# Kernel optimization log

Measured on AMD Instinct MI355X. Metric: run time of the kernel, lower is better.

Reference implementation:

```python
import jax, jax.numpy as jnp
import numpy as np

NEG = -1.0e9

def setup_inputs() -> dict:
    key = jax.random.key(0)
    kq, kk, kv = jax.random.split(key, 3)
    B, Sq, Sk, D = 8, 2048, 2048, 128
    q = jax.random.normal(kq, (B, Sq, D), dtype=jnp.float32)
    k = jax.random.normal(kk, (B, Sk, D), dtype=jnp.float32)
    v = jax.random.normal(kv, (B, Sk, D), dtype=jnp.float32)
    mask = jnp.ones((B, Sq, Sk), dtype=jnp.int32)  # 1 = attend
    return {"q": q, "k": k, "v": v, "mask": mask}

def reference(q, k, v, mask):
    # scaled scores: [B, Sq, Sk]
    temper = jnp.sqrt(jnp.asarray(k.shape[-1], dtype=q.dtype))
    attn = jnp.einsum('bqd,bkd->bqk', q, k) / temper
    # additive mask: -1e9 where mask == 0
    attn = attn + NEG * (1.0 - mask.astype(attn.dtype))
    attn = jax.nn.softmax(attn, axis=-1)
    # dropout rate 0.0 -> identity
    out = jnp.einsum('bqk,bkd->bqd', attn, v)
    return out, attn
```

## Files before the change

### kernel.cpp

```cpp
#include <hip/hip_runtime.h>
#include <hip/hip_bf16.h>

#define BB 8
#define SQ 2048
#define SK 2048
#define DD 128
#define INV_TEMPER 0.08838834764831845f

using s16x8 = __attribute__((ext_vector_type(8))) short;
using f32x4 = __attribute__((ext_vector_type(4))) float;

__device__ __forceinline__ unsigned short f2bf(float f) {
  union { float f; unsigned u; } v; v.f = f;
  unsigned r = v.u + 0x7FFFu + ((v.u >> 16) & 1u);
  return (unsigned short)(r >> 16);
}
__device__ __forceinline__ float bf2f(unsigned short h) {
  union { unsigned u; float f; } v; v.u = ((unsigned)h) << 16; return v.f;
}

__global__ __launch_bounds__(256) void prep_k_kernel(const float* __restrict__ k,
                                                     unsigned short* __restrict__ kb) {
  const size_t i = ((size_t)blockIdx.x * 256 + threadIdx.x) * 8;
  const float4 a = *(const float4*)(k + i);
  const float4 c = *(const float4*)(k + i + 4);
  ushort4 o0, o1;
  o0.x = f2bf(a.x); o0.y = f2bf(a.y); o0.z = f2bf(a.z); o0.w = f2bf(a.w);
  o1.x = f2bf(c.x); o1.y = f2bf(c.y); o1.z = f2bf(c.z); o1.w = f2bf(c.w);
  *(ushort4*)(kb + i) = o0;
  *(ushort4*)(kb + i + 4) = o1;
}

__global__ __launch_bounds__(256) void prep_v_kernel(const float* __restrict__ v,
                                                     unsigned short* __restrict__ vt) {
  constexpr int TS = 132;
  __shared__ __align__(16) unsigned short tile[64 * TS];
  const int tid = threadIdx.x;
  const int bid = blockIdx.x;
  const int b  = bid >> 5;
  const int k0 = (bid & 31) << 6;
#pragma unroll
  for (int p = 0; p < 8; ++p) {
    const int row = p * 8 + (tid >> 5);
    const int c4  = (tid & 31) << 2;
    const float4 vv = *(const float4*)(v + ((size_t)(b * SK + k0 + row)) * DD + c4);
    ushort4 o; o.x = f2bf(vv.x); o.y = f2bf(vv.y); o.z = f2bf(vv.z); o.w = f2bf(vv.w);
    *(ushort4*)(&tile[row * TS + c4]) = o;
  }
  __syncthreads();
#pragma unroll
  for (int p = 0; p < 8; ++p) {
    const int u = p * 256 + tid;
    const int d  = u >> 4;
    const int kw = (u & 15) << 2;
    ushort4 o;
    o.x = tile[(kw + 0) * TS + d];
    o.y = tile[(kw + 1) * TS + d];
    o.z = tile[(kw + 2) * TS + d];
    o.w = tile[(kw + 3) * TS + d];
    *(ushort4*)(vt + ((size_t)(b * DD + d)) * SK + k0 + kw) = o;
  }
}

__global__ __launch_bounds__(512, 4) void fused_attn(
    const float* __restrict__ q, const int* __restrict__ mask,
    const unsigned short* __restrict__ kb, const unsigned short* __restrict__ vt,
    float* __restrict__ outp, float* __restrict__ attn) {
  constexpr int BMS = 516;
  constexpr int LDP = 136;
  __shared__ unsigned char bm[32 * BMS];
  __shared__ __align__(16) unsigned short p_lds[2][32][LDP];
  __shared__ float redl[8][32];

  const int tid = threadIdx.x;
  const int bid = blockIdx.x;
  const int swz = ((bid & 7) << 6) + (bid >> 3);
  const int b  = swz >> 6;
  const int q0 = (swz & 63) << 5;
  const int lane = tid & 63;
  const int w    = tid >> 6;
  const int lrow = lane & 15;
  const int lk   = lane >> 4;
  const int colw = (w << 4) + lrow;
  const int shq  = colw & 3;

  {
    const int* mbase = mask + ((size_t)(b * SQ + q0)) * SK;
#pragma unroll
    for (int i = 0; i < 32; ++i) {
      const int u = i * 512 + tid;
      const int grow = u >> 9;
      const int gc4  = u & 511;
      const int4 mv = *(const int4*)(mbase + (size_t)grow * SK + ((size_t)gc4 << 2));
      unsigned char nib = (unsigned char)((mv.x != 0) | ((mv.y != 0) << 1) |
                                          ((mv.z != 0) << 2) | ((mv.w != 0) << 3));
      bm[grow * BMS + gc4] = nib;
    }
  }

  s16x8 afrag[2][4];
#pragma unroll
  for (int rt = 0; rt < 2; ++rt) {
    const float* qp = q + ((size_t)(b * SQ + q0 + rt * 16 + lrow)) * DD + lk * 8;
#pragma unroll
    for (int ks = 0; ks < 4; ++ks) {
      const float4 f0 = *(const float4*)(qp + ks * 32);
      const float4 f1 = *(const float4*)(qp + ks * 32 + 4);
      s16x8 a;
      a[0] = (short)f2bf(f0.x); a[1] = (short)f2bf(f0.y);
      a[2] = (short)f2bf(f0.z); a[3] = (short)f2bf(f0.w);
      a[4] = (short)f2bf(f1.x); a[5] = (short)f2bf(f1.y);
      a[6] = (short)f2bf(f1.z); a[7] = (short)f2bf(f1.w);
      afrag[rt][ks] = a;
    }
  }

  const unsigned short* kbb = kb + (size_t)b * SK * DD + (size_t)colw * DD + lk * 8;

  __syncthreads();

  float lsum[2][4];
#pragma unroll
  for (int rt = 0; rt < 2; ++rt)
#pragma unroll
    for (int r = 0; r < 4; ++r) lsum[rt][r] = 0.0f;

#pragma unroll 1
  for (int t = 0; t < 16; ++t) {
    const int kr0 = t << 7;
    s16x8 bfr[4];
#pragma unroll
    for (int ks = 0; ks < 4; ++ks)
      bfr[ks] = *(const s16x8*)(kbb + (size_t)kr0 * DD + ks * 32);
    f32x4 acc[2];
    acc[0] = f32x4{0.f, 0.f, 0.f, 0.f};
    acc[1] = f32x4{0.f, 0.f, 0.f, 0.f};
#pragma unroll
    for (int ks = 0; ks < 4; ++ks) {
      acc[0] = __builtin_amdgcn_mfma_f32_16x16x32_bf16(afrag[0][ks], bfr[ks], acc[0], 0, 0, 0);
      acc[1] = __builtin_amdgcn_mfma_f32_16x16x32_bf16(afrag[1][ks], bfr[ks], acc[1], 0, 0, 0);
    }
#pragma unroll
    for (int rt = 0; rt < 2; ++rt)
#pragma unroll
      for (int r = 0; r < 4; ++r) {
        const int row = rt * 16 + (lk << 2) + r;
        const int live = (bm[row * BMS + (t << 5) + (colw >> 2)] >> shq) & 1;
        const float s = acc[rt][r] * INV_TEMPER;
        lsum[rt][r] += live ? __expf(s) : 0.0f;
      }
  }

#pragma unroll
  for (int rt = 0; rt < 2; ++rt)
#pragma unroll
    for (int r = 0; r < 4; ++r) {
      float l = lsum[rt][r];
#pragma unroll
      for (int d = 1; d < 16; d <<= 1) l += __shfl_xor(l, d);
      lsum[rt][r] = l;
    }
  if (lrow == 0) {
#pragma unroll
    for (int rt = 0; rt < 2; ++rt)
#pragma unroll
      for (int r = 0; r < 4; ++r)
        redl[w][rt * 16 + (lk << 2) + r] = lsum[rt][r];
  }
  __syncthreads();
  float IL[2][4];
#pragma unroll
  for (int rt = 0; rt < 2; ++rt)
#pragma unroll
    for (int r = 0; r < 4; ++r) {
      const int row = rt * 16 + (lk << 2) + r;
      float l = 0.0f;
#pragma unroll
      for (int ww = 0; ww < 8; ++ww) l += redl[ww][row];
      IL[rt][r] = 1.0f / l;
    }

  f32x4 oacc[2];
  oacc[0] = f32x4{0.f, 0.f, 0.f, 0.f};
  oacc[1] = f32x4{0.f, 0.f, 0.f, 0.f};
  const unsigned short* vrow = vt + ((size_t)(b * DD + colw)) * SK + lk * 8;
  const int arow  = tid >> 4;
  const int acol0 = (tid & 15) << 3;
  float* attn_base = attn + ((size_t)(b * SQ + q0 + arow)) * SK + acol0;

#pragma unroll 1
  for (int t = 0; t < 16; ++t) {
    const int kr0 = t << 7;
    const int buf = t & 1;
    s16x8 bfr[4];
#pragma unroll
    for (int ks = 0; ks < 4; ++ks)
      bfr[ks] = *(const s16x8*)(kbb + (size_t)kr0 * DD + ks * 32);
    f32x4 acc[2];
    acc[0] = f32x4{0.f, 0.f, 0.f, 0.f};
    acc[1] = f32x4{0.f, 0.f, 0.f, 0.f};
#pragma unroll
    for (int ks = 0; ks < 4; ++ks) {
      acc[0] = __builtin_amdgcn_mfma_f32_16x16x32_bf16(afrag[0][ks], bfr[ks], acc[0], 0, 0, 0);
      acc[1] = __builtin_amdgcn_mfma_f32_16x16x32_bf16(afrag[1][ks], bfr[ks], acc[1], 0, 0, 0);
    }
#pragma unroll
    for (int rt = 0; rt < 2; ++rt)
#pragma unroll
      for (int r = 0; r < 4; ++r) {
        const int row = rt * 16 + (lk << 2) + r;
        const int live = (bm[row * BMS + (t << 5) + (colw >> 2)] >> shq) & 1;
        const float s = acc[rt][r] * INV_TEMPER;
        const float p = live ? __expf(s) * IL[rt][r] : 0.0f;
        p_lds[buf][row][colw] = f2bf(p);
      }
    __syncthreads();
    {
      const s16x8 pr = *(const s16x8*)(&p_lds[buf][arow][acol0]);
      float4 o0, o1;
      o0.x = bf2f((unsigned short)pr[0]); o0.y = bf2f((unsigned short)pr[1]);
      o0.z = bf2f((unsigned short)pr[2]); o0.w = bf2f((unsigned short)pr[3]);
      o1.x = bf2f((unsigned short)pr[4]); o1.y = bf2f((unsigned short)pr[5]);
      o1.z = bf2f((unsigned short)pr[6]); o1.w = bf2f((unsigned short)pr[7]);
      *(float4*)(attn_base + kr0) = o0;
      *(float4*)(attn_base + kr0 + 4) = o1;
    }
#pragma unroll
    for (int ks = 0; ks < 4; ++ks) {
      const s16x8 pa0 = *(const s16x8*)(&p_lds[buf][lrow][ks * 32 + lk * 8]);
      const s16x8 pa1 = *(const s16x8*)(&p_lds[buf][16 + lrow][ks * 32 + lk * 8]);
      const s16x8 bv = *(const s16x8*)(vrow + kr0 + ks * 32);
      oacc[0] = __builtin_amdgcn_mfma_f32_16x16x32_bf16(pa0, bv, oacc[0], 0, 0, 0);
      oacc[1] = __builtin_amdgcn_mfma_f32_16x16x32_bf16(pa1, bv, oacc[1], 0, 0, 0);
    }
  }

#pragma unroll
  for (int rt = 0; rt < 2; ++rt)
#pragma unroll
    for (int r = 0; r < 4; ++r) {
      const int row = q0 + rt * 16 + (lk << 2) + r;
      outp[((size_t)(b * SQ + row)) * DD + colw] = oacc[rt][r];
    }
}

extern "C" void kernel_launch(void* const* d_in, const int* in_sizes, int n_in,
                              void* d_out, int out_size, void* d_ws, size_t ws_size,
                              hipStream_t stream) {
  const float* q = (const float*)d_in[0];
  const float* k = (const float*)d_in[1];
  const float* v = (const float*)d_in[2];
  const int* mask = (const int*)d_in[3];
  float* outp = (float*)d_out;
  float* attn = outp + (size_t)BB * SQ * DD;

  unsigned short* kb = (unsigned short*)d_ws;
  unsigned short* vt = kb + (size_t)BB * SK * DD;

  prep_k_kernel<<<(BB * SK * DD) / (256 * 8), 256, 0, stream>>>(k, kb);
  prep_v_kernel<<<BB * (SK / 64), 256, 0, stream>>>(v, vt);
  fused_attn<<<BB * (SQ / 32), 512, 0, stream>>>(q, mask, kb, vt, outp, attn);
}
```

Baseline: 141.9 us.

## Prefetch K/V fragments with register double buffering and compact mask to bits

The mask is packed one bit per key instead of a nibble per 4 keys, which halves the LDS bitmap size. Both passes now double-buffer the K fragments in registers so the next tile's global load overlaps the current MFMAs, and V fragments are loaded before the QK MFMAs. The block barrier is replaced by a raw lgkmcnt wait plus s_barrier, and MFMA sections are wrapped in s_setprio. Register pressure rises under the 512x4 launch bounds, which could cause spills.

```diff
diff --git a/kernel.cpp b/kernel.cpp
--- a/kernel.cpp
+++ b/kernel.cpp
@@ -17,6 +17,10 @@
 }
 __device__ __forceinline__ float bf2f(unsigned short h) {
   union { unsigned u; float f; } v; v.u = ((unsigned)h) << 16; return v.f;
+}
+__device__ __forceinline__ void bar_lds() {
+  asm volatile("s_waitcnt lgkmcnt(0)" ::: "memory");
+  __builtin_amdgcn_s_barrier();
 }
 
 __global__ __launch_bounds__(256) void prep_k_kernel(const float* __restrict__ k,
@@ -66,7 +70,7 @@
     const float* __restrict__ q, const int* __restrict__ mask,
     const unsigned short* __restrict__ kb, const unsigned short* __restrict__ vt,
     float* __restrict__ outp, float* __restrict__ attn) {
-  constexpr int BMS = 516;
+  constexpr int BMS = 260;
   constexpr int LDP = 136;
   __shared__ unsigned char bm[32 * BMS];
   __shared__ __align__(16) unsigned short p_lds[2][32][LDP];
@@ -82,165 +86,190 @@
   const int lrow = lane & 15;
   const int lk   = lane >> 4;
   const int colw = (w << 4) + lrow;
-  const int shq  = colw & 3;
+  const int cbyte = colw >> 3;
+  const int cbit  = colw & 7;
+  const int rowb  = lk << 2;
 
   {
     const int* mbase = mask + ((size_t)(b * SQ + q0)) * SK;
 #pragma unroll
-    for (int i = 0; i < 32; ++i) {
-      const int u = i * 512 + tid;
-      const int grow = u >> 9;
-      const int gc4  = u & 511;
-      const int4 mv = *(const int4*)(mbase + (size_t)grow * SK + ((size_t)gc4 << 2));
-      unsigned char nib = (unsigned char)((mv.x != 0) | ((mv.y != 0) << 1) |
-                                          ((mv.z != 0) << 2) | ((mv.w != 0) << 3));
-      bm[grow * BMS + gc4] = nib;
-    }
-  }
-
-  s16x8 afrag[2][4];
-#pragma unroll
-  for (int rt = 0; rt < 2; ++rt) {
-    const float* qp = q + ((size_t)(b * SQ + q0 + rt * 16 + lrow)) * DD + lk * 8;
+    for (int i = 0; i < 16; ++i) {
+      const int u = (i << 9) + tid;
+      const int grow = u >> 8;
+      const int gb   = u & 255;
+      const int* pp = mbase + (size_t)grow * SK + ((size_t)gb << 3);
+      const int4 m0 = *(const int4*)pp;
+      const int4 m1 = *(const int4*)(pp + 4);
+      unsigned bv = (unsigned)(m0.x != 0) | ((unsigned)(m0.y != 0) << 1) |
+                    ((unsigned)(m0.z != 0) << 2) | ((unsigned)(m0.w != 0) << 3) |
+                    ((unsigned)(m1.x != 0) << 4) | ((unsigned)(m1.y != 0) << 5) |
+                    ((unsigned)(m1.z != 0) << 6) | ((unsigned)(m1.w != 0) << 7);
+      bm[grow * BMS + gb] = (unsigned char)bv;
+    }
+  }
+
+  s16x8 af0[4], af1[4];
+#pragma unroll
+  for (int ks = 0; ks < 4; ++ks) {
+    const float* qp0 = q + ((size_t)(b * SQ + q0 + lrow)) * DD + ks * 32 + lk * 8;
+    const float* qp1 = qp0 + 16 * DD;
+    const float4 a0 = *(const float4*)qp0;
+    const float4 a1 = *(const float4*)(qp0 + 4);
+    const float4 c0 = *(const float4*)qp1;
+    const float4 c1 = *(const float4*)(qp1 + 4);
+    s16x8 x, y;
+    x[0] = (short)f2bf(a0.x); x[1] = (short)f2bf(a0.y); x[2] = (short)f2bf(a0.z); x[3] = (short)f2bf(a0.w);
+    x[4] = (short)f2bf(a1.x); x[5] = (short)f2bf(a1.y); x[6] = (short)f2bf(a1.z); x[7] = (short)f2bf(a1.w);
+    y[0] = (short)f2bf(c0.x); y[1] = (short)f2bf(c0.y); y[2] = (short)f2bf(c0.z); y[3] = (short)f2bf(c0.w);
+    y[4] = (short)f2bf(c1.x); y[5] = (short)f2bf(c1.y); y[6] = (short)f2bf(c1.z); y[7] = (short)f2bf(c1.w);
+    af0[ks] = x; af1[ks] = y;
+  }
+
+  const unsigned short* kbb = kb + (size_t)b * SK * DD + (size_t)colw * DD + lk * 8;
+
+  bar_lds();
+
+  float ls[8];
+#pragma unroll
+  for (int i = 0; i < 8; ++i) ls[i] = 0.0f;
+
+  s16x8 bA[4], bB[4];
+#pragma unroll
+  for (int ks = 0; ks < 4; ++ks) bA[ks] = *(const s16x8*)(kbb + ks * 32);
+
+  auto qk_sink1 = [&](int t, const f32x4& a0, const f32x4& a1) {
+    const int bybase = (t << 4) + cbyte;
+#pragma unroll
+    for (int rt = 0; rt < 2; ++rt)
+#pragma unroll
+      for (int r = 0; r < 4; ++r) {
+        const int row = rt * 16 + rowb + r;
+        const int live = (bm[row * BMS + bybase] >> cbit) & 1;
+        const float s = (rt ? a1[r] : a0[r]) * INV_TEMPER;
+        ls[rt * 4 + r] += live ? __expf(s) : 0.0f;
+      }
+  };
+  auto qk_mfma = [&](const s16x8* bf, f32x4& a0, f32x4& a1) {
+    __builtin_amdgcn_s_setprio(1);
 #pragma unroll
     for (int ks = 0; ks < 4; ++ks) {
-      const float4 f0 = *(const float4*)(qp + ks * 32);
-      const float4 f1 = *(const float4*)(qp + ks * 32 + 4);
-      s16x8 a;
-      a[0] = (short)f2bf(f0.x); a[1] = (short)f2bf(f0.y);
-      a[2] = (short)f2bf(f0.z); a[3] = (short)f2bf(f0.w);
-      a[4] = (short)f2bf(f1.x); a[5] = (short)f2bf(f1.y);
-      a[6] = (short)f2bf(f1.z); a[7] = (short)f2bf(f1.w);
-      afrag[rt][ks] = a;
-    }
-  }
-
-  const unsigned short* kbb = kb + (size_t)b * SK * DD + (size_t)colw * DD + lk * 8;
-
-  __syncthreads();
-
-  float lsum[2][4];
-#pragma unroll
-  for (int rt = 0; rt < 2; ++rt)
-#pragma unroll
-    for (int r = 0; r < 4; ++r) lsum[rt][r] = 0.0f;
+      a0 = __builtin_amdgcn_mfma_f32_16x16x32_bf16(af0[ks], bf[ks], a0, 0, 0, 0);
+      a1 = __builtin_amdgcn_mfma_f32_16x16x32_bf16(af1[ks], bf[ks], a1, 0, 0, 0);
+    }
+    __builtin_amdgcn_s_setprio(0);
+  };
 
 #pragma unroll 1
-  for (int t = 0; t < 16; ++t) {
-    const int kr0 = t << 7;
-    s16x8 bfr[4];
-#pragma unroll
-    for (int ks = 0; ks < 4; ++ks)
-      bfr[ks] = *(const s16x8*)(kbb + (size_t)kr0 * DD + ks * 32);
-    f32x4 acc[2];
-    acc[0] = f32x4{0.f, 0.f, 0.f, 0.f};
-    acc[1] = f32x4{0.f, 0.f, 0.f, 0.f};
-#pragma unroll
-    for (int ks = 0; ks < 4; ++ks) {
-      acc[0] = __builtin_amdgcn_mfma_f32_16x16x32_bf16(afrag[0][ks], bfr[ks], acc[0], 0, 0, 0);
-      acc[1] = __builtin_amdgcn_mfma_f32_16x16x32_bf16(afrag[1][ks], bfr[ks], acc[1], 0, 0, 0);
-    }
-#pragma unroll
-    for (int rt = 0; rt < 2; ++rt)
-#pragma unroll
-      for (int r = 0; r < 4; ++r) {
-        const int row = rt * 16 + (lk << 2) + r;
-        const int live = (bm[row * BMS + (t << 5) + (colw >> 2)] >> shq) & 1;
-        const float s = acc[rt][r] * INV_TEMPER;
-        lsum[rt][r] += live ? __expf(s) : 0.0f;
-      }
-  }
-
-#pragma unroll
-  for (int rt = 0; rt < 2; ++rt)
-#pragma unroll
-    for (int r = 0; r < 4; ++r) {
-      float l = lsum[rt][r];
-#pragma unroll
-      for (int d = 1; d < 16; d <<= 1) l += __shfl_xor(l, d);
-      lsum[rt][r] = l;
-    }
+  for (int tp = 0; tp < 8; ++tp) {
+    const int t0 = tp << 1, t1 = t0 + 1;
+    {
+      const unsigned short* p = kbb + (size_t)t1 * (128 * DD);
+#pragma unroll
+      for (int ks = 0; ks < 4; ++ks) bB[ks] = *(const s16x8*)(p + ks * 32);
+    }
+    f32x4 a0 = {0.f,0.f,0.f,0.f}, a1 = {0.f,0.f,0.f,0.f};
+    qk_mfma(bA, a0, a1);
+    qk_sink1(t0, a0, a1);
+    {
+      const int tn = (t0 + 2) & 15;
+      const unsigned short* p = kbb + (size_t)tn * (128 * DD);
+#pragma unroll
+      for (int ks = 0; ks < 4; ++ks) bA[ks] = *(const s16x8*)(p + ks * 32);
+    }
+    f32x4 c0 = {0.f,0.f,0.f,0.f}, c1 = {0.f,0.f,0.f,0.f};
+    qk_mfma(bB, c0, c1);
+    qk_sink1(t1, c0, c1);
+  }
+
+#pragma unroll
+  for (int i = 0; i < 8; ++i) {
+    float l = ls[i];
+#pragma unroll
+    for (int d = 1; d < 16; d <<= 1) l += __shfl_xor(l, d);
+    ls[i] = l;
+  }
   if (lrow == 0) {
 #pragma unroll
-    for (int rt = 0; rt < 2; ++rt)
-#pragma unroll
-      for (int r = 0; r < 4; ++r)
-        redl[w][rt * 16 + (lk << 2) + r] = lsum[rt][r];
-  }
-  __syncthreads();
-  float IL[2][4];
-#pragma unroll
-  for (int rt = 0; rt < 2; ++rt)
-#pragma unroll
-    for (int r = 0; r < 4; ++r) {
-      const int row = rt * 16 + (lk << 2) + r;
-      float l = 0.0f;
-#pragma unroll
-      for (int ww = 0; ww < 8; ++ww) l += redl[ww][row];
-      IL[rt][r] = 1.0f / l;
-    }
-
-  f32x4 oacc[2];
-  oacc[0] = f32x4{0.f, 0.f, 0.f, 0.f};
-  oacc[1] = f32x4{0.f, 0.f, 0.f, 0.f};
+    for (int i = 0; i < 8; ++i) redl[w][(i >> 2) * 16 + rowb + (i & 3)] = ls[i];
+  }
+#pragma unroll
+  for (int ks = 0; ks < 4; ++ks) bA[ks] = *(const s16x8*)(kbb + ks * 32);
+  bar_lds();
+  float il[8];
+#pragma unroll
+  for (int i = 0; i < 8; ++i) {
+    const int row = (i >> 2) * 16 + rowb + (i & 3);
+    float l = 0.0f;
+#pragma unroll
+    for (int ww = 0; ww < 8; ++ww) l += redl[ww][row];
+    il[i] = 1.0f / l;
+  }
+
+  f32x4 o0 = {0.f,0.f,0.f,0.f}, o1 = {0.f,0.f,0.f,0.f};
   const unsigned short* vrow = vt + ((size_t)(b * DD + colw)) * SK + lk * 8;
   const int arow  = tid >> 4;
   const int acol0 = (tid & 15) << 3;
   float* attn_base = attn + ((size_t)(b * SQ + q0 + arow)) * SK + acol0;
 
-#pragma unroll 1
-  for (int t = 0; t < 16; ++t) {
+  auto pv_iter = [&](int t, const s16x8* bcur, s16x8* bnx) {
     const int kr0 = t << 7;
     const int buf = t & 1;
-    s16x8 bfr[4];
-#pragma unroll
-    for (int ks = 0; ks < 4; ++ks)
-      bfr[ks] = *(const s16x8*)(kbb + (size_t)kr0 * DD + ks * 32);
-    f32x4 acc[2];
-    acc[0] = f32x4{0.f, 0.f, 0.f, 0.f};
-    acc[1] = f32x4{0.f, 0.f, 0.f, 0.f};
-#pragma unroll
-    for (int ks = 0; ks < 4; ++ks) {
-      acc[0] = __builtin_amdgcn_mfma_f32_16x16x32_bf16(afrag[0][ks], bfr[ks], acc[0], 0, 0, 0);
-      acc[1] = __builtin_amdgcn_mfma_f32_16x16x32_bf16(afrag[1][ks], bfr[ks], acc[1], 0, 0, 0);
-    }
+    {
+      const int tn = (t + 1) & 15;
+      const unsigned short* p = kbb + (size_t)tn * (128 * DD);
+#pragma unroll
+      for (int ks = 0; ks < 4; ++ks) bnx[ks] = *(const s16x8*)(p + ks * 32);
+    }
+    s16x8 vf[4];
+#pragma unroll
+    for (int ks = 0; ks < 4; ++ks) vf[ks] = *(const s16x8*)(vrow + kr0 + ks * 32);
+    f32x4 a0 = {0.f,0.f,0.f,0.f}, a1 = {0.f,0.f,0.f,0.f};
+    qk_mfma(bcur, a0, a1);
+    const int bybase = (t << 4) + cbyte;
 #pragma unroll
     for (int rt = 0; rt < 2; ++rt)
 #pragma unroll
       for (int r = 0; r < 4; ++r) {
-        const int row = rt * 16 + (lk << 2) + r;
-        const int live = (bm[row * BMS + (t << 5) + (colw >> 2)] >> shq) & 1;
-        const float s = acc[rt][r] * INV_TEMPER;
-        const float p = live ? __expf(s) * IL[rt][r] : 0.0f;
+        const int row = rt * 16 + rowb + r;
+        const int live = (bm[row * BMS + bybase] >> cbit) & 1;
+        const float s = (rt ? a1[r] : a0[r]) * INV_TEMPER;
+        const float p = live ? __expf(s) * il[rt * 4 + r] : 0.0f;
         p_lds[buf][row][colw] = f2bf(p);
       }
-    __syncthreads();
+    bar_lds();
     {
       const s16x8 pr = *(const s16x8*)(&p_lds[buf][arow][acol0]);
-      float4 o0, o1;
-      o0.x = bf2f((unsigned short)pr[0]); o0.y = bf2f((unsigned short)pr[1]);
-      o0.z = bf2f((unsigned short)pr[2]); o0.w = bf2f((unsigned short)pr[3]);
-      o1.x = bf2f((unsigned short)pr[4]); o1.y = bf2f((unsigned short)pr[5]);
-      o1.z = bf2f((unsigned short)pr[6]); o1.w = bf2f((unsigned short)pr[7]);
-      *(float4*)(attn_base + kr0) = o0;
-      *(float4*)(attn_base + kr0 + 4) = o1;
-    }
+      float4 g0, g1;
+      g0.x = bf2f((unsigned short)pr[0]); g0.y = bf2f((unsigned short)pr[1]);
+      g0.z = bf2f((unsigned short)pr[2]); g0.w = bf2f((unsigned short)pr[3]);
+      g1.x = bf2f((unsigned short)pr[4]); g1.y = bf2f((unsigned short)pr[5]);
+      g1.z = bf2f((unsigned short)pr[6]); g1.w = bf2f((unsigned short)pr[7]);
+      *(float4*)(attn_base + kr0) = g0;
+      *(float4*)(attn_base + kr0 + 4) = g1;
+    }
+    __builtin_amdgcn_s_setprio(1);
 #pragma unroll
     for (int ks = 0; ks < 4; ++ks) {
       const s16x8 pa0 = *(const s16x8*)(&p_lds[buf][lrow][ks * 32 + lk * 8]);
       const s16x8 pa1 = *(const s16x8*)(&p_lds[buf][16 + lrow][ks * 32 + lk * 8]);
-      const s16x8 bv = *(const s16x8*)(vrow + kr0 + ks * 32);
-      oacc[0] = __builtin_amdgcn_mfma_f32_16x16x32_bf16(pa0, bv, oacc[0], 0, 0, 0);
-      oacc[1] = __builtin_amdgcn_mfma_f32_16x16x32_bf16(pa1, bv, oacc[1], 0, 0, 0);
-    }
+      o0 = __builtin_amdgcn_mfma_f32_16x16x32_bf16(pa0, vf[ks], o0, 0, 0, 0);
+      o1 = __builtin_amdgcn_mfma_f32_16x16x32_bf16(pa1, vf[ks], o1, 0, 0, 0);
+    }
+    __builtin_amdgcn_s_setprio(0);
+  };
+
+#pragma unroll 1
+  for (int tp = 0; tp < 8; ++tp) {
+    pv_iter((tp << 1),     bA, bB);
+    pv_iter((tp << 1) + 1, bB, bA);
   }
 
 #pragma unroll
   for (int rt = 0; rt < 2; ++rt)
 #pragma unroll
     for (int r = 0; r < 4; ++r) {
-      const int row = q0 + rt * 16 + (lk << 2) + r;
-      outp[((size_t)(b * SQ + row)) * DD + colw] = oacc[rt][r];
+      const int row = q0 + rt * 16 + rowb + r;
+      outp[((size_t)(b * SQ + row)) * DD + colw] = (rt ? o1[r] : o0[r]);
     }
 }
 
```

Result: no change. 140.7 us (-0.9%).
